# Kernel tuning notes

Hardware: AMD Instinct MI355X
Metric: run time of the kernel (lower is better)

Reference implementation:

```python
import jax, jax.numpy as jnp
import numpy as np

B, S, D, H, MEM, P = 32, 512, 768, 8, 768, 3
DK = D // H
LN_EPS = 1e-6


def _layer_norm(x, a, b):
    # torch LayerNorm in source uses unbiased std (ddof=1) and adds eps to std
    mean = x.mean(-1, keepdims=True)
    var = ((x - mean) ** 2).sum(-1, keepdims=True) / (x.shape[-1] - 1)
    return a * (x - mean) / (jnp.sqrt(var) + LN_EPS) + b


def _gcn_branch(x, mask, Wq, bq, Wk, bk, Ws, bs):
    # x: [B,S,D], mask: [B,S] 0/1 ints
    q = (x @ Wq.T + bq).reshape(B, S, H, DK).transpose(0, 2, 1, 3)  # [B,H,S,DK]
    k = (x @ Wk.T + bk).reshape(B, S, H, DK).transpose(0, 2, 1, 3)
    scores = jnp.einsum('bhqd,bhkd->bhqk', q, k) / jnp.sqrt(jnp.float32(DK))
    scores = jnp.where(mask[:, None, None, :] == 0, jnp.float32(-1e9), scores)
    adj = jax.nn.softmax(scores, axis=-1).mean(1)  # average heads -> [B,S,S]
    # adj - diag(diag(adj)) + I  ==  set diagonal to 1
    idx = jnp.arange(S)
    adj = adj.at[:, idx, idx].set(1.0)
    adj = adj * mask[:, :, None].astype(adj.dtype)  # src_mask.transpose(1,2) * adj
    denom = adj.sum(-1, keepdims=True) + 1.0
    out = x
    for W, b in zip(Ws, bs):
        out = jax.nn.relu((adj @ out @ W.T + b) / denom)
    return out, adj


def _proj(a, b):
    # Proj(a, b): (a.b / |b|) * normalize(b)
    b_mo = jnp.sqrt((b * b).sum(-1))
    axb = (a * b).sum(-1)
    bn = b / jnp.maximum(jnp.sqrt((b * b).sum(-1, keepdims=True)), 1e-12)
    return (axb / b_mo)[:, None] * bn


def setup_inputs() -> dict:
    key = jax.random.key(0)
    ks = jax.random.split(key, 32)

    def w(k, shape):
        return jax.random.normal(k, shape, jnp.float32) * 0.02

    inp = {
        'sequence_output': jax.random.normal(ks[0], (B, S, D), jnp.float32),
        'pooled_output': jax.random.normal(ks[1], (B, D), jnp.float32),
        'src_mask': jnp.ones((B, S), jnp.int32),
        'aspect_mask': jnp.ones((B, S), jnp.float32),
        'ln_a': jnp.ones((D,), jnp.float32),
        'ln_b': jnp.zeros((D,), jnp.float32),
        'fp_Wq': w(ks[2], (D, D)), 'fp_bq': jnp.zeros((D,), jnp.float32),
        'fp_Wk': w(ks[3], (D, D)), 'fp_bk': jnp.zeros((D,), jnp.float32),
        'fp_W0': w(ks[4], (MEM, D)), 'fp_b0': jnp.zeros((MEM,), jnp.float32),
        'fp_W1': w(ks[5], (MEM, MEM)), 'fp_b1': jnp.zeros((MEM,), jnp.float32),
        'fc_Wq': w(ks[6], (D, D)), 'fc_bq': jnp.zeros((D,), jnp.float32),
        'fc_Wk': w(ks[7], (D, D)), 'fc_bk': jnp.zeros((D,), jnp.float32),
        'fc_W0': w(ks[8], (MEM, D)), 'fc_b0': jnp.zeros((MEM,), jnp.float32),
        'fc_W1': w(ks[9], (MEM, MEM)), 'fc_b1': jnp.zeros((MEM,), jnp.float32),
        'fp_dense_W': w(ks[10], (P, MEM)), 'fp_dense_b': jnp.zeros((P,), jnp.float32),
        'fc_dense_W': w(ks[11], (P, MEM)), 'fc_dense_b': jnp.zeros((P,), jnp.float32),
    }
    return inp


def reference(sequence_output, pooled_output, src_mask, aspect_mask,
              ln_a, ln_b,
              fp_Wq, fp_bq, fp_Wk, fp_bk, fp_W0, fp_b0, fp_W1, fp_b1,
              fc_Wq, fc_bq, fc_Wk, fc_bk, fc_W0, fc_b0, fc_W1, fc_b1,
              fp_dense_W, fp_dense_b, fc_dense_W, fc_dense_b):
    label_embedding = pooled_output
    att_inputs = _layer_norm(sequence_output, ln_a, ln_b)  # dropout disabled (eval)
    asp_wn = aspect_mask.sum(1)[:, None]  # [B,1]

    fp_out, _ = _gcn_branch(att_inputs, src_mask, fp_Wq, fp_bq, fp_Wk, fp_bk,
                            [fp_W0, fp_W1], [fp_b0, fp_b1])
    fc_out, _ = _gcn_branch(att_inputs, src_mask, fc_Wq, fc_bq, fc_Wk, fc_bk,
                            [fc_W0, fc_W1], [fc_b0, fc_b1])

    outputs_fp = fp_out.sum(1)  # [B,MEM]
    outputs_fc = (fc_out * aspect_mask[:, :, None]).sum(1) / asp_wn  # [B,MEM]

    fp_x = _proj(outputs_fp, outputs_fc)
    fp_y = _proj(outputs_fp, outputs_fp - fp_x)
    fc_y = outputs_fc  # gradient-reverse layer is identity in forward

    logits_p = fp_y @ fp_dense_W.T + fp_dense_b
    logits_c = fc_y @ fc_dense_W.T + fc_dense_b
    return (logits_p, logits_c, fp_y, label_embedding)
```

## Files before the change

### kernel.cpp

```cpp
#include <hip/hip_runtime.h>
#include <math.h>
#include <stdint.h>

#define Bn 32
#define Sn 512
#define Dn 768
#define Hn 8
#define DKn 96
#define Pn 3

typedef __bf16 bf16_t;
typedef bf16_t bf16x8 __attribute__((ext_vector_type(8)));
typedef float f32x4 __attribute__((ext_vector_type(4)));

__device__ __forceinline__ bf16_t f2bf(float f) { return (bf16_t)f; }

__device__ __forceinline__ void gload16(const void* g, void* l) {
    __builtin_amdgcn_global_load_lds((const __attribute__((address_space(1))) void*)g,
                                     (__attribute__((address_space(3))) void*)l, 16, 0, 0);
}

__device__ __forceinline__ float brsum(float v, float* red) {
    int t = threadIdx.x;
    red[t] = v; __syncthreads();
    #pragma unroll
    for (int o = 128; o > 0; o >>= 1) {
        if (t < o) red[t] += red[t + o];
        __syncthreads();
    }
    float r = red[0]; __syncthreads();
    return r;
}

__global__ __launch_bounds__(256) void ln_kernel(const float* __restrict__ in,
                                                 const float* __restrict__ ga,
                                                 const float* __restrict__ gb,
                                                 bf16_t* __restrict__ out) {
    __shared__ float red[256];
    long row = blockIdx.x;
    const float* x = in + row * Dn;
    bf16_t* y = out + row * Dn;
    int t = threadIdx.x;
    float v0 = x[t], v1 = x[t + 256], v2 = x[t + 512];
    float mean = brsum(v0 + v1 + v2, red) / (float)Dn;
    float d0 = v0 - mean, d1 = v1 - mean, d2 = v2 - mean;
    float ss = brsum(d0 * d0 + d1 * d1 + d2 * d2, red);
    float inv = 1.0f / (sqrtf(ss / (float)(Dn - 1)) + 1e-6f);
    y[t]       = f2bf(ga[t]       * d0 * inv + gb[t]);
    y[t + 256] = f2bf(ga[t + 256] * d1 * inv + gb[t + 256]);
    y[t + 512] = f2bf(ga[t + 512] * d2 * inv + gb[t + 512]);
}

__global__ __launch_bounds__(256) void cvt8(const float* __restrict__ s0,
                                            const float* __restrict__ s1,
                                            const float* __restrict__ s2,
                                            const float* __restrict__ s3,
                                            const float* __restrict__ s4,
                                            const float* __restrict__ s5,
                                            const float* __restrict__ s6,
                                            const float* __restrict__ s7,
                                            bf16_t* __restrict__ dst) {
    int y = blockIdx.y;
    const float* s = (y == 0) ? s0 : (y == 1) ? s1 : (y == 2) ? s2 : (y == 3) ? s3
                   : (y == 4) ? s4 : (y == 5) ? s5 : (y == 6) ? s6 : s7;
    long i = (long)blockIdx.x * 1024 + threadIdx.x * 4;
    float4 v = *reinterpret_cast<const float4*>(s + i);
    bf16_t* d = dst + (long)y * Dn * Dn + i;
    d[0] = f2bf(v.x); d[1] = f2bf(v.y); d[2] = f2bf(v.z); d[3] = f2bf(v.w);
}

__global__ __launch_bounds__(256) void biascat_k(const float* __restrict__ s0,
                                                 const float* __restrict__ s1,
                                                 const float* __restrict__ s2,
                                                 const float* __restrict__ s3,
                                                 const float* __restrict__ s4,
                                                 const float* __restrict__ s5,
                                                 const float* __restrict__ s6,
                                                 const float* __restrict__ s7,
                                                 float* __restrict__ dst) {
    int y = blockIdx.x;
    const float* s = (y == 0) ? s0 : (y == 1) ? s1 : (y == 2) ? s2 : (y == 3) ? s3
                   : (y == 4) ? s4 : (y == 5) ? s5 : (y == 6) ? s6 : s7;
    for (int i = threadIdx.x; i < Dn; i += 256) dst[(long)y * Dn + i] = s[i];
}

__global__ void zero_kernel(float* p, int n) {
    int i = blockIdx.x * 256 + threadIdx.x;
    if (i < n) p[i] = 0.0f;
}

template <int EPI>
__global__ __launch_bounds__(256) void gemm_bt(
    const bf16_t* __restrict__ Ag, const bf16_t* __restrict__ Bg,
    bf16_t* __restrict__ Cg, float* __restrict__ outv,
    int lda, int ldb, int ldc, int K,
    long sAhi, long sAlo, long sBhi, long sBlo, long sChi, long sClo,
    int lgZ, float alpha,
    const float* __restrict__ bias, long bias_zs,
    const float* __restrict__ denom,
    const float* __restrict__ aspw) {
    __shared__ __align__(16) bf16_t As[128 * 32];
    __shared__ __align__(16) bf16_t Bs[128 * 32];

    unsigned gx = gridDim.x, gy = gridDim.y;
    unsigned nwg = gx * gy * gridDim.z;
    unsigned flat = (blockIdx.z * gy + blockIdx.y) * gx + blockIdx.x;
    unsigned q8 = nwg >> 3, r8 = nwg & 7;
    unsigned xcd = flat & 7, idx = flat >> 3;
    unsigned swz = (xcd < r8 ? xcd * (q8 + 1) : r8 * (q8 + 1) + (xcd - r8) * q8) + idx;
    unsigned bx = swz % gx;
    unsigned rest = swz / gx;
    unsigned by = rest % gy;
    unsigned zz = rest / gy;
    int zb = zz >> lgZ;
    int zg = zz & ((1 << lgZ) - 1);
    long zful = zz;

    const bf16_t* A = Ag + zb * sAhi + zg * sAlo;
    const bf16_t* B = Bg + zb * sBhi + zg * sBlo;

    int n0 = bx * 128;
    int m0 = by * 128;
    int tid = threadIdx.x;
    int lane = tid & 63, wv = tid >> 6;
    int wm = wv >> 1, wn = wv & 1;

    int sub = lane >> 2;
    int kcol = (lane & 3) * 8;
    const bf16_t* pA0 = A + (size_t)(m0 + wv * 16 + sub) * lda + kcol;
    const bf16_t* pA1 = pA0 + (size_t)64 * lda;
    const bf16_t* pB0 = B + (size_t)(n0 + wv * 16 + sub) * ldb + kcol;
    const bf16_t* pB1 = pB0 + (size_t)64 * ldb;
    bf16_t* lA0 = As + wv * 512 + lane * 8;
    bf16_t* lA1 = As + (4 + wv) * 512 + lane * 8;
    bf16_t* lB0 = Bs + wv * 512 + lane * 8;
    bf16_t* lB1 = Bs + (4 + wv) * 512 + lane * 8;

    f32x4 acc[4][4];
    #pragma unroll
    for (int i = 0; i < 4; i++)
        #pragma unroll
        for (int j = 0; j < 4; j++) acc[i][j] = (f32x4){0.f, 0.f, 0.f, 0.f};

    const bf16_t* ar = As + (wm * 64 + (lane & 15)) * 32 + (lane >> 4) * 8;
    const bf16_t* br = Bs + (wn * 64 + (lane & 15)) * 32 + (lane >> 4) * 8;

    for (int k0 = 0; k0 < K; k0 += 32) {
        gload16(pA0 + k0, lA0);
        gload16(pA1 + k0, lA1);
        gload16(pB0 + k0, lB0);
        gload16(pB1 + k0, lB1);
        __syncthreads();
        bf16x8 a[4], b[4];
        #pragma unroll
        for (int i = 0; i < 4; i++) a[i] = *(const bf16x8*)(ar + i * 16 * 32);
        #pragma unroll
        for (int j = 0; j < 4; j++) b[j] = *(const bf16x8*)(br + j * 16 * 32);
        #pragma unroll
        for (int i = 0; i < 4; i++)
            #pragma unroll
            for (int j = 0; j < 4; j++)
                acc[i][j] = __builtin_amdgcn_mfma_f32_16x16x32_bf16(a[i], b[j], acc[i][j], 0, 0, 0);
        __syncthreads();
    }

    int nb = n0 + wn * 64 + (lane & 15);
    int mbase = m0 + wm * 64 + (lane >> 4) * 4;
    const float* bz = bias ? bias + zb * bias_zs : nullptr;

    if (EPI == 0) {
        bf16_t* Cz = Cg + zb * sChi + zg * sClo;
        #pragma unroll
        for (int i = 0; i < 4; i++) {
            #pragma unroll
            for (int r = 0; r < 4; r++) {
                long m = mbase + i * 16 + r;
                bf16_t* crow = Cz + m * (long)ldc;
                #pragma unroll
                for (int j = 0; j < 4; j++) {
                    int col = nb + j * 16;
                    float v = acc[i][j][r] * alpha;
                    if (bz) v += bz[col];
                    crow[col] = f2bf(v);
                }
            }
        }
    } else if (EPI == 1) {
        bf16_t* Cz = Cg + zb * sChi + zg * sClo;
        const float* dz = denom + zful * Sn;
        #pragma unroll
        for (int i = 0; i < 4; i++) {
            #pragma unroll
            for (int r = 0; r < 4; r++) {
                int m = mbase + i * 16 + r;
                float dinv = 1.0f / dz[m];
                bf16_t* crow = Cz + (long)m * ldc;
                #pragma unroll
                for (int j = 0; j < 4; j++) {
                    float v = fmaxf((acc[i][j][r] + bz[nb + j * 16]) * dinv, 0.0f);
                    crow[nb + j * 16] = f2bf(v);
                }
            }
        }
    } else {
        const float* dz = denom + zful * Sn;
        float csum[4] = {0.f, 0.f, 0.f, 0.f};
        #pragma unroll
        for (int i = 0; i < 4; i++) {
            #pragma unroll
            for (int r = 0; r < 4; r++) {
                int m = mbase + i * 16 + r;
                float dinv = 1.0f / dz[m];
                float wgt = (aspw && zb) ? aspw[(long)zg * Sn + m] : 1.0f;
                #pragma unroll
                for (int j = 0; j < 4; j++) {
                    float v = fmaxf((acc[i][j][r] + bz[nb + j * 16]) * dinv, 0.0f);
                    csum[j] += v * wgt;
                }
            }
        }
        #pragma unroll
        for (int j = 0; j < 4; j++) {
            float s = csum[j];
            s += __shfl_xor(s, 16);
            s += __shfl_xor(s, 32);
            if (lane < 16) atomicAdd(&outv[zful * Dn + nb + j * 16], s);
        }
    }
}

template <int EPI>
__global__ __launch_bounds__(512, 1) void gemm256(
    const bf16_t* __restrict__ Ag, const bf16_t* __restrict__ Bg,
    bf16_t* __restrict__ Cg, float* __restrict__ outv,
    int lda, int ldb, int ldc, int K,
    long sAhi, long sAlo, long sBhi, long sBlo, long sChi, long sClo,
    int lgZ,
    const float* __restrict__ bias, long bias_zs,
    const float* __restrict__ denom,
    const float* __restrict__ aspw) {
    __shared__ __align__(16) bf16_t lds[4][2][8192];

    unsigned gx = gridDim.x, gy = gridDim.y;
    unsigned nwg = gx * gy * gridDim.z;
    unsigned flat = (blockIdx.z * gy + blockIdx.y) * gx + blockIdx.x;
    unsigned q8 = nwg >> 3, r8 = nwg & 7;
    unsigned xcd = flat & 7, idx = flat >> 3;
    unsigned swz = (xcd < r8 ? xcd * (q8 + 1) : r8 * (q8 + 1) + (xcd - r8) * q8) + idx;
    unsigned bx = swz % gx;
    unsigned rest = swz / gx;
    unsigned by = rest % gy;
    unsigned zz = rest / gy;
    int zb = zz >> lgZ;
    int zg = zz & ((1 << lgZ) - 1);
    long zful = zz;

    const bf16_t* A = Ag + zb * sAhi + zg * sAlo;
    const bf16_t* B = Bg + zb * sBhi + zg * sBlo;

    int n0 = bx * 256, m0 = by * 256;
    int tid = threadIdx.x;
    int lane = tid & 63, w = tid >> 6;
    int wm = w >> 2, wn = w & 3;

    const int NT = K >> 5;

    int srow = lane & 15;
    int skc = (lane >> 4) * 8;
    const bf16_t* Asrc0 = A + (size_t)(m0 + (w * 2 + 0) * 16 + srow) * lda + skc;
    const bf16_t* Asrc1 = A + (size_t)(m0 + (w * 2 + 1) * 16 + srow) * lda + skc;
    const bf16_t* Bsrc0 = B + (size_t)(n0 + (w * 2 + 0) * 16 + srow) * ldb + skc;
    const bf16_t* Bsrc1 = B + (size_t)(n0 + (w * 2 + 1) * 16 + srow) * ldb + skc;
    int c0off = (w * 2 + 0) * 512 + lane * 8;
    int c1off = (w * 2 + 1) * 512 + lane * 8;

    f32x4 acc[8][4];
    #pragma unroll
    for (int i = 0; i < 8; ++i)
        #pragma unroll
        for (int j = 0; j < 4; ++j) acc[i][j] = (f32x4){0.f, 0.f, 0.f, 0.f};

    #pragma unroll
    for (int tt = 0; tt < 3; ++tt) {
        gload16(Asrc0 + tt * 32, &lds[tt][0][c0off]);
        gload16(Asrc1 + tt * 32, &lds[tt][0][c1off]);
        gload16(Bsrc0 + tt * 32, &lds[tt][1][c0off]);
        gload16(Bsrc1 + tt * 32, &lds[tt][1][c1off]);
    }
    asm volatile("s_waitcnt vmcnt(8)" ::: "memory");
    __builtin_amdgcn_s_barrier();

    int aoff = wm * 8 * 512 + lane * 8;
    int boff = wn * 4 * 512 + lane * 8;

    for (int t = 0; t < NT; ++t) {
        const bf16_t* bufA = &lds[t & 3][0][0];
        const bf16_t* bufB = &lds[t & 3][1][0];
        int tn = t + 3;
        bf16_t* dA = &lds[tn & 3][0][0];
        bf16_t* dB = &lds[tn & 3][1][0];
        bool st = tn < NT;

        bf16x8 a[4], b[4];
        #pragma unroll
        for (int i = 0; i < 4; ++i)
            a[i] = *(const bf16x8*)(bufA + aoff + i * 512);
        #pragma unroll
        for (int j = 0; j < 4; ++j)
            b[j] = *(const bf16x8*)(bufB + boff + j * 512);
        if (st) {
            gload16(Asrc0 + tn * 32, dA + c0off);
            gload16(Bsrc0 + tn * 32, dB + c0off);
        }
        __builtin_amdgcn_s_barrier();
        asm volatile("s_waitcnt lgkmcnt(0)" ::: "memory");
        __builtin_amdgcn_sched_barrier(0);
        __builtin_amdgcn_s_setprio(1);
        #pragma unroll
        for (int i = 0; i < 4; ++i)
            #pragma unroll
            for (int j = 0; j < 4; ++j)
                acc[i][j] = __builtin_amdgcn_mfma_f32_16x16x32_bf16(a[i], b[j], acc[i][j], 0, 0, 0);
        __builtin_amdgcn_s_setprio(0);
        __builtin_amdgcn_s_barrier();

        #pragma unroll
        for (int i = 0; i < 4; ++i)
            a[i] = *(const bf16x8*)(bufA + aoff + (4 + i) * 512);
        if (st) {
            gload16(Asrc1 + tn * 32, dA + c1off);
            gload16(Bsrc1 + tn * 32, dB + c1off);
        }
        __builtin_amdgcn_s_barrier();
        asm volatile("s_waitcnt lgkmcnt(0)" ::: "memory");
        __builtin_amdgcn_sched_barrier(0);
        __builtin_amdgcn_s_setprio(1);
        #pragma unroll
        for (int i = 0; i < 4; ++i)
            #pragma unroll
            for (int j = 0; j < 4; ++j)
                acc[4 + i][j] = __builtin_amdgcn_mfma_f32_16x16x32_bf16(a[i], b[j], acc[4 + i][j], 0, 0, 0);
        __builtin_amdgcn_s_setprio(0);
        if (t + 3 < NT)      asm volatile("s_waitcnt vmcnt(8)" ::: "memory");
        else if (t + 2 < NT) asm volatile("s_waitcnt vmcnt(4)" ::: "memory");
        else                 asm volatile("s_waitcnt vmcnt(0)" ::: "memory");
        __builtin_amdgcn_s_barrier();
    }

    int nb = n0 + wn * 64 + (lane & 15);
    int mbase = m0 + wm * 128 + (lane >> 4) * 4;
    const float* bz = bias ? bias + zb * bias_zs : nullptr;

    if (EPI == 0) {
        bf16_t* Cz = Cg + zb * sChi + zg * sClo;
        #pragma unroll
        for (int i = 0; i < 8; ++i) {
            #pragma unroll
            for (int r = 0; r < 4; ++r) {
                long m = mbase + i * 16 + r;
                bf16_t* crow = Cz + m * (long)ldc;
                #pragma unroll
                for (int j = 0; j < 4; ++j) {
                    int col = nb + j * 16;
                    float v = acc[i][j][r];
                    if (bz) v += bz[col];
                    crow[col] = f2bf(v);
                }
            }
        }
    }
}

__global__ __launch_bounds__(256, 2) void fused_adj(
    const bf16_t* __restrict__ QK, bf16_t* __restrict__ adjb,
    float* __restrict__ denomv, const int* __restrict__ mask) {
    __shared__ __align__(16) bf16_t stg[32 * 520];
    __shared__ float red[4][16];

    int L = blockIdx.x;
    int swzi = (L & 7) * 128 + (L >> 3);
    int brc = swzi >> 9;
    int rem = swzi & 511;
    int b = rem >> 4;
    int q0 = (rem & 15) * 32;

    int tid = threadIdx.x;
    int lane = tid & 63, w = tid >> 6;
    int mt = w >> 1, nh = w & 1;
    int g = lane >> 4, c = lane & 15;

    const long LDQ = 3072;
    const bf16_t* Qrow = QK + ((long)b * Sn + q0 + mt * 16 + c) * LDQ + brc * 1536 + g * 8;
    const bf16_t* Kbase = QK + ((long)b * Sn + nh * 64 + c) * LDQ + brc * 1536 + Dn + g * 8;

    const int* mrow = mask + (long)b * Sn;
    unsigned mbits = 0;
    #pragma unroll
    for (int t = 0; t < 4; ++t)
        #pragma unroll
        for (int nj = 0; nj < 4; ++nj)
            if (mrow[t * 128 + nh * 64 + nj * 16 + c] != 0) mbits |= 1u << (t * 4 + nj);

    f32x4 adjacc[4][4];
    #pragma unroll
    for (int t = 0; t < 4; ++t)
        #pragma unroll
        for (int nj = 0; nj < 4; ++nj) adjacc[t][nj] = (f32x4){0.f, 0.f, 0.f, 0.f};

    bf16x8 krA[6], krB[6], aq[3], aqn[3];
    const float sal = 0.102062072615966f;

    #pragma unroll
    for (int jj = 0; jj < 2; ++jj)
        #pragma unroll
        for (int ks = 0; ks < 3; ++ks)
            krA[jj * 3 + ks] = *(const bf16x8*)(Kbase + (long)(jj * 16) * LDQ + ks * 32);
    #pragma unroll
    for (int ks = 0; ks < 3; ++ks)
        aq[ks] = *(const bf16x8*)(Qrow + ks * 32);

    for (int h = 0; h < Hn; ++h) {
        f32x4 S[4][4];
        #pragma unroll
        for (int t = 0; t < 4; ++t)
            #pragma unroll
            for (int nj = 0; nj < 4; ++nj) S[t][nj] = (f32x4){0.f, 0.f, 0.f, 0.f};

        #pragma unroll
        for (int ht = 0; ht < 8; ++ht) {
            const int t = ht >> 1, half = ht & 1;
            const int nht = (ht + 1) & 7;
            const int hinc = (ht == 7) ? 1 : 0;
            const int t2 = nht >> 1, half2 = nht & 1;
            const bf16_t* kb2 = Kbase + (long)(t2 * 128) * LDQ + (long)(h + hinc) * 96;
            if ((ht & 1) == 0) {
                #pragma unroll
                for (int jj = 0; jj < 2; ++jj)
                    #pragma unroll
                    for (int ks = 0; ks < 3; ++ks)
                        krB[jj * 3 + ks] = *(const bf16x8*)(kb2 + (long)((half2 * 2 + jj) * 16) * LDQ + ks * 32);
            } else {
                #pragma unroll
                for (int jj = 0; jj < 2; ++jj)
                    #pragma unroll
                    for (int ks = 0; ks < 3; ++ks)
                        krA[jj * 3 + ks] = *(const bf16x8*)(kb2 + (long)((half2 * 2 + jj) * 16) * LDQ + ks * 32);
            }
            if (ht == 6) {
                #pragma unroll
                for (int ks = 0; ks < 3; ++ks)
                    aqn[ks] = *(const bf16x8*)(Qrow + (long)(h + 1) * 96 + ks * 32);
            }
            if ((ht & 1) == 0) {
                #pragma unroll
                for (int jj = 0; jj < 2; ++jj)
                    #pragma unroll
                    for (int ks = 0; ks < 3; ++ks)
                        S[t][half * 2 + jj] = __builtin_amdgcn_mfma_f32_16x16x32_bf16(
                            aq[ks], krA[jj * 3 + ks], S[t][half * 2 + jj], 0, 0, 0);
            } else {
                #pragma unroll
                for (int jj = 0; jj < 2; ++jj)
                    #pragma unroll
                    for (int ks = 0; ks < 3; ++ks)
                        S[t][half * 2 + jj] = __builtin_amdgcn_mfma_f32_16x16x32_bf16(
                            aq[ks], krB[jj * 3 + ks], S[t][half * 2 + jj], 0, 0, 0);
            }
        }

        float rs[4] = {0.f, 0.f, 0.f, 0.f};
        #pragma unroll
        for (int t = 0; t < 4; ++t)
            #pragma unroll
            for (int nj = 0; nj < 4; ++nj) {
                float mkf = ((mbits >> (t * 4 + nj)) & 1u) ? 1.0f : 0.0f;
                #pragma unroll
                for (int ri = 0; ri < 4; ++ri) {
                    float e = mkf * __expf(S[t][nj][ri] * sal);
                    S[t][nj][ri] = e;
                    rs[ri] += e;
                }
            }
        #pragma unroll
        for (int ri = 0; ri < 4; ++ri) {
            rs[ri] += __shfl_xor(rs[ri], 1);
            rs[ri] += __shfl_xor(rs[ri], 2);
            rs[ri] += __shfl_xor(rs[ri], 4);
            rs[ri] += __shfl_xor(rs[ri], 8);
        }
        if (c == 0) {
            #pragma unroll
            for (int ri = 0; ri < 4; ++ri) red[w][g * 4 + ri] = rs[ri];
        }
        __syncthreads();
        float inv[4];
        #pragma unroll
        for (int ri = 0; ri < 4; ++ri)
            inv[ri] = 0.125f / (red[w][g * 4 + ri] + red[w ^ 1][g * 4 + ri]);
        __syncthreads();
        #pragma unroll
        for (int t = 0; t < 4; ++t)
            #pragma unroll
            for (int nj = 0; nj < 4; ++nj)
                #pragma unroll
                for (int ri = 0; ri < 4; ++ri)
                    adjacc[t][nj][ri] += S[t][nj][ri] * inv[ri];
        if (h < 7) {
            #pragma unroll
            for (int ks = 0; ks < 3; ++ks) aq[ks] = aqn[ks];
        }
    }

    float rm[4];
    #pragma unroll
    for (int ri = 0; ri < 4; ++ri)
        rm[ri] = (mrow[q0 + mt * 16 + g * 4 + ri] != 0) ? 1.0f : 0.0f;
    float rs2[4] = {0.f, 0.f, 0.f, 0.f};
    #pragma unroll
    for (int t = 0; t < 4; ++t)
        #pragma unroll
        for (int nj = 0; nj < 4; ++nj) {
            int n = t * 128 + nh * 64 + nj * 16 + c;
            #pragma unroll
            for (int ri = 0; ri < 4; ++ri) {
                float v = adjacc[t][nj][ri];
                int q = q0 + mt * 16 + g * 4 + ri;
                if (n == q) v = 1.0f;
                v *= rm[ri];
                adjacc[t][nj][ri] = v;
                rs2[ri] += v;
            }
        }
    #pragma unroll
    for (int ri = 0; ri < 4; ++ri) {
        rs2[ri] += __shfl_xor(rs2[ri], 1);
        rs2[ri] += __shfl_xor(rs2[ri], 2);
        rs2[ri] += __shfl_xor(rs2[ri], 4);
        rs2[ri] += __shfl_xor(rs2[ri], 8);
    }
    if (c == 0) {
        #pragma unroll
        for (int ri = 0; ri < 4; ++ri) red[w][g * 4 + ri] = rs2[ri];
    }
    __syncthreads();
    long zful = (long)brc * Bn + b;
    if (nh == 0 && c == 0) {
        #pragma unroll
        for (int ri = 0; ri < 4; ++ri)
            denomv[zful * Sn + q0 + mt * 16 + g * 4 + ri] =
                red[w][g * 4 + ri] + red[w ^ 1][g * 4 + ri] + 1.0f;
    }
    #pragma unroll
    for (int t = 0; t < 4; ++t)
        #pragma unroll
        for (int nj = 0; nj < 4; ++nj) {
            int n = t * 128 + nh * 64 + nj * 16 + c;
            #pragma unroll
            for (int ri = 0; ri < 4; ++ri)
                stg[(mt * 16 + g * 4 + ri) * 520 + n] = f2bf(adjacc[t][nj][ri]);
        }
    __syncthreads();
    bf16_t* arow = adjb + (zful * Sn + q0) * Sn;
    #pragma unroll
    for (int p = 0; p < 8; ++p) {
        int gr = tid + p * 256;
        int row = gr >> 6, cc = gr & 63;
        *(bf16x8*)(arow + (long)row * Sn + cc * 8) = *(const bf16x8*)(stg + row * 520 + cc * 8);
    }
}

__global__ __launch_bounds__(256) void final_kernel(const float* __restrict__ ofp,
                                                    const float* __restrict__ ofc_raw,
                                                    const float* __restrict__ aspect,
                                                    const float* __restrict__ pooled,
                                                    const float* __restrict__ fpdW,
                                                    const float* __restrict__ fpdb,
                                                    const float* __restrict__ fcdW,
                                                    const float* __restrict__ fcdb,
                                                    float* __restrict__ out) {
    __shared__ float red[256];
    __shared__ float fp[Dn], fc[Dn], fy[Dn];
    int b = blockIdx.x, t = threadIdx.x;
    float awv = aspect[(long)b * Sn + t] + aspect[(long)b * Sn + t + 256];
    float asp_wn = brsum(awv, red);
    for (int i = t; i < Dn; i += 256) {
        fp[i] = ofp[(long)b * Dn + i];
        fc[i] = ofc_raw[(long)b * Dn + i] / asp_wn;
    }
    __syncthreads();
    float p0 = 0.0f, p1 = 0.0f;
    for (int i = t; i < Dn; i += 256) { p0 += fc[i] * fc[i]; p1 += fp[i] * fc[i]; }
    float dfc2 = brsum(p0, red);
    float dfpfc = brsum(p1, red);
    float bmo = sqrtf(dfc2);
    float coef = dfpfc / bmo;
    float bden = fmaxf(bmo, 1e-12f);
    float q0 = 0.0f, q1 = 0.0f;
    for (int i = t; i < Dn; i += 256) {
        float tv = fp[i] - coef * fc[i] / bden;
        fy[i] = tv;
        q0 += tv * tv;
        q1 += fp[i] * tv;
    }
    float dt2 = brsum(q0, red);
    float dfpt = brsum(q1, red);
    float tmo = sqrtf(dt2);
    float coef2 = dfpt / tmo;
    float tden = fmaxf(tmo, 1e-12f);
    for (int i = t; i < Dn; i += 256) fy[i] = coef2 * fy[i] / tden;
    __syncthreads();
    for (int i = t; i < Dn; i += 256) out[2 * Bn * Pn + (long)b * Dn + i] = fy[i];
    for (int i = t; i < Dn; i += 256)
        out[2 * Bn * Pn + Bn * Dn + (long)b * Dn + i] = pooled[(long)b * Dn + i];
    for (int j = 0; j < Pn; j++) {
        float lp = 0.0f, lc = 0.0f;
        for (int i = t; i < Dn; i += 256) {
            lp += fy[i] * fpdW[(long)j * Dn + i];
            lc += fc[i] * fcdW[(long)j * Dn + i];
        }
        float rp = brsum(lp, red);
        float rc = brsum(lc, red);
        if (t == 0) {
            out[(long)b * Pn + j] = rp + fpdb[j];
            out[Bn * Pn + (long)b * Pn + j] = rc + fcdb[j];
        }
    }
}

extern "C" void kernel_launch(void* const* d_in, const int* in_sizes, int n_in,
                              void* d_out, int out_size, void* d_ws, size_t ws_size,
                              hipStream_t stream) {
    const float* seq     = (const float*)d_in[0];
    const float* pooled  = (const float*)d_in[1];
    const int*   src_msk = (const int*)d_in[2];
    const float* aspect  = (const float*)d_in[3];
    const float* ln_a    = (const float*)d_in[4];
    const float* ln_b    = (const float*)d_in[5];
    float* out = (float*)d_out;

    const long NTD = (long)Bn * Sn * Dn;
    const long NSS = (long)Bn * Sn * Sn;
    const long DD  = (long)Dn * Dn;
    const long SD  = (long)Sn * Dn;

    char* w = (char*)d_ws;
    bf16_t* xbf   = (bf16_t*)w;
    bf16_t* QK    = xbf + NTD;
    bf16_t* H1    = QK;
    bf16_t* XT    = QK + 2 * NTD;
    bf16_t* adjb  = QK + 4 * NTD;
    float*  denom = (float*)(adjb + 2 * NSS);
    float*  ofp   = denom + 2L * Bn * Sn;
    float*  bcat  = ofp + 2L * Bn * Dn;
    bf16_t* Wb    = (bf16_t*)(bcat + 8 * Dn);

    ln_kernel<<<dim3(Bn * Sn), dim3(256), 0, stream>>>(seq, ln_a, ln_b, xbf);
    zero_kernel<<<dim3((2 * Bn * Dn + 255) / 256), dim3(256), 0, stream>>>(ofp, 2 * Bn * Dn);

    cvt8<<<dim3(576, 8), dim3(256), 0, stream>>>(
        (const float*)d_in[6], (const float*)d_in[8],
        (const float*)d_in[14], (const float*)d_in[16],
        (const float*)d_in[10], (const float*)d_in[18],
        (const float*)d_in[12], (const float*)d_in[20], Wb);
    biascat_k<<<dim3(8), dim3(256), 0, stream>>>(
        (const float*)d_in[7], (const float*)d_in[9],
        (const float*)d_in[15], (const float*)d_in[17],
        (const float*)d_in[11], (const float*)d_in[19],
        (const float*)d_in[13], (const float*)d_in[21], bcat);

    gemm256<0><<<dim3(12, 64, 1), dim3(512), 0, stream>>>(
        xbf, Wb, QK, nullptr, Dn, Dn, 3072, Dn,
        0, 0, 0, 0, 0, 0, 0, bcat, 0, nullptr, nullptr);

    fused_adj<<<dim3(2 * Bn * Sn / 32), dim3(256), 0, stream>>>(QK, adjb, denom, src_msk);

    gemm_bt<0><<<dim3(4, 6, 64), dim3(256), 0, stream>>>(
        Wb + 4 * DD, xbf, XT, nullptr, Dn, Dn, Sn, Dn,
        DD, 0, 0, SD, 32 * SD, SD,
        5, 1.0f, nullptr, 0, nullptr, nullptr);

    gemm_bt<1><<<dim3(6, 4, 64), dim3(256), 0, stream>>>(
        adjb, XT, H1, nullptr, Sn, Sn, Dn, Sn,
        32L * Sn * Sn, (long)Sn * Sn, 32 * SD, SD, 32 * SD, SD,
        5, 1.0f, bcat + 4 * Dn, Dn, denom, nullptr);

    gemm_bt<0><<<dim3(4, 6, 64), dim3(256), 0, stream>>>(
        Wb + 6 * DD, H1, XT, nullptr, Dn, Dn, Sn, Dn,
        DD, 0, 32 * SD, SD, 32 * SD, SD,
        5, 1.0f, nullptr, 0, nullptr, nullptr);

    gemm_bt<2><<<dim3(6, 4, 64), dim3(256), 0, stream>>>(
        adjb, XT, nullptr, ofp, Sn, Sn, 0, Sn,
        32L * Sn * Sn, (long)Sn * Sn, 32 * SD, SD, 0, 0,
        5, 1.0f, bcat + 6 * Dn, Dn, denom, aspect);

    final_kernel<<<dim3(Bn), dim3(256), 0, stream>>>(
        ofp, ofp + (long)Bn * Dn, aspect, pooled,
        (const float*)d_in[22], (const float*)d_in[23],
        (const float*)d_in[24], (const float*)d_in[25], out);
}
```

Before: 566.4 us.

## Stage K tiles through double-buffered LDS in fused_adj with 512-thread blocks

The fused adjacency kernel used to have each wave load its own K fragments straight from global memory into registers. It now loads each 128-row K tile for a head cooperatively into a padded, double-buffered LDS buffer, prefetching two tiles ahead in registers. Blocks grow from 4 to 8 waves, each covering 32 key columns instead of 64, and the row-sum reduction now spans four waves. This is meant to cut redundant global K loads and raise occupancy, at the cost of a __syncthreads per tile and extra LDS traffic.

Result: slower. 654.6 us (median of 3 runs) (+15.6%).

```diff
diff --git a/kernel.cpp b/kernel.cpp
--- a/kernel.cpp
+++ b/kernel.cpp
@@ -253,7 +253,6 @@
     unsigned zz = rest / gy;
     int zb = zz >> lgZ;
     int zg = zz & ((1 << lgZ) - 1);
-    long zful = zz;
 
     const bf16_t* A = Ag + zb * sAhi + zg * sAlo;
     const bf16_t* B = Bg + zb * sBhi + zg * sBlo;
@@ -371,11 +370,11 @@
     }
 }
 
-__global__ __launch_bounds__(256, 2) void fused_adj(
+__global__ __launch_bounds__(512, 4) void fused_adj(
     const bf16_t* __restrict__ QK, bf16_t* __restrict__ adjb,
     float* __restrict__ denomv, const int* __restrict__ mask) {
-    __shared__ __align__(16) bf16_t stg[32 * 520];
-    __shared__ float red[4][16];
+    __shared__ __align__(16) bf16_t shmem[2 * 128 * 100];
+    __shared__ float red[8][16];
 
     int L = blockIdx.x;
     int swzi = (L & 7) * 128 + (L >> 3);
@@ -386,128 +385,139 @@
 
     int tid = threadIdx.x;
     int lane = tid & 63, w = tid >> 6;
-    int mt = w >> 1, nh = w & 1;
+    int mt = w >> 2, nh = w & 3;
     int g = lane >> 4, c = lane & 15;
 
     const long LDQ = 3072;
     const bf16_t* Qrow = QK + ((long)b * Sn + q0 + mt * 16 + c) * LDQ + brc * 1536 + g * 8;
-    const bf16_t* Kbase = QK + ((long)b * Sn + nh * 64 + c) * LDQ + brc * 1536 + Dn + g * 8;
+    const bf16_t* Kst  = QK + (long)b * Sn * LDQ + brc * 1536 + Dn;
 
     const int* mrow = mask + (long)b * Sn;
     unsigned mbits = 0;
     #pragma unroll
     for (int t = 0; t < 4; ++t)
         #pragma unroll
-        for (int nj = 0; nj < 4; ++nj)
-            if (mrow[t * 128 + nh * 64 + nj * 16 + c] != 0) mbits |= 1u << (t * 4 + nj);
-
-    f32x4 adjacc[4][4];
+        for (int grp = 0; grp < 2; ++grp)
+            if (mrow[t * 128 + nh * 32 + grp * 16 + c] != 0) mbits |= 1u << (t * 2 + grp);
+
+    int sr[3], sc[3];
+    #pragma unroll
+    for (int p = 0; p < 3; ++p) { int ci = tid + p * 512; sr[p] = ci / 12; sc[p] = (ci % 12) * 8; }
+
+    bf16_t* Ks0 = shmem;
+    bf16_t* Ks1 = shmem + 128 * 100;
+
+    f32x4 adjacc[4][2];
     #pragma unroll
     for (int t = 0; t < 4; ++t)
         #pragma unroll
-        for (int nj = 0; nj < 4; ++nj) adjacc[t][nj] = (f32x4){0.f, 0.f, 0.f, 0.f};
-
-    bf16x8 krA[6], krB[6], aq[3], aqn[3];
+        for (int grp = 0; grp < 2; ++grp) adjacc[t][grp] = (f32x4){0.f, 0.f, 0.f, 0.f};
+
+    bf16x8 krA[3], krB[3];
     const float sal = 0.102062072615966f;
 
     #pragma unroll
-    for (int jj = 0; jj < 2; ++jj)
+    for (int p = 0; p < 3; ++p)
+        krA[p] = *(const bf16x8*)(Kst + (long)sr[p] * LDQ + sc[p]);
+    #pragma unroll
+    for (int p = 0; p < 3; ++p)
+        *(bf16x8*)(Ks0 + sr[p] * 100 + sc[p]) = krA[p];
+    #pragma unroll
+    for (int p = 0; p < 3; ++p)
+        krB[p] = *(const bf16x8*)(Kst + (long)(128 + sr[p]) * LDQ + sc[p]);
+    __syncthreads();
+
+    int koff = (nh * 32 + c) * 100 + g * 8;
+
+    for (int h = 0; h < Hn; ++h) {
+        f32x4 S[4][2];
+        #pragma unroll
+        for (int t = 0; t < 4; ++t)
+            #pragma unroll
+            for (int grp = 0; grp < 2; ++grp) S[t][grp] = (f32x4){0.f, 0.f, 0.f, 0.f};
+        bf16x8 aq[3];
         #pragma unroll
         for (int ks = 0; ks < 3; ++ks)
-            krA[jj * 3 + ks] = *(const bf16x8*)(Kbase + (long)(jj * 16) * LDQ + ks * 32);
-    #pragma unroll
-    for (int ks = 0; ks < 3; ++ks)
-        aq[ks] = *(const bf16x8*)(Qrow + ks * 32);
-
-    for (int h = 0; h < Hn; ++h) {
-        f32x4 S[4][4];
-        #pragma unroll
-        for (int t = 0; t < 4; ++t)
-            #pragma unroll
-            for (int nj = 0; nj < 4; ++nj) S[t][nj] = (f32x4){0.f, 0.f, 0.f, 0.f};
-
-        #pragma unroll
-        for (int ht = 0; ht < 8; ++ht) {
-            const int t = ht >> 1, half = ht & 1;
-            const int nht = (ht + 1) & 7;
-            const int hinc = (ht == 7) ? 1 : 0;
-            const int t2 = nht >> 1, half2 = nht & 1;
-            const bf16_t* kb2 = Kbase + (long)(t2 * 128) * LDQ + (long)(h + hinc) * 96;
-            if ((ht & 1) == 0) {
-                #pragma unroll
-                for (int jj = 0; jj < 2; ++jj)
+            aq[ks] = *(const bf16x8*)(Qrow + (long)h * 96 + ks * 32);
+
+        #pragma unroll
+        for (int t = 0; t < 4; ++t) {
+            int it = h * 4 + t;
+            if (it + 2 < 32) {
+                int i2 = it + 2, t2 = i2 & 3, h2 = i2 >> 2;
+                const bf16_t* kb = Kst + (long)(t2 * 128) * LDQ + h2 * 96;
+                if ((it & 1) == 0) {
                     #pragma unroll
-                    for (int ks = 0; ks < 3; ++ks)
-                        krB[jj * 3 + ks] = *(const bf16x8*)(kb2 + (long)((half2 * 2 + jj) * 16) * LDQ + ks * 32);
-            } else {
-                #pragma unroll
-                for (int jj = 0; jj < 2; ++jj)
+                    for (int p = 0; p < 3; ++p)
+                        krA[p] = *(const bf16x8*)(kb + (long)sr[p] * LDQ + sc[p]);
+                } else {
                     #pragma unroll
-                    for (int ks = 0; ks < 3; ++ks)
-                        krA[jj * 3 + ks] = *(const bf16x8*)(kb2 + (long)((half2 * 2 + jj) * 16) * LDQ + ks * 32);
-            }
-            if (ht == 6) {
-                #pragma unroll
-                for (int ks = 0; ks < 3; ++ks)
-                    aqn[ks] = *(const bf16x8*)(Qrow + (long)(h + 1) * 96 + ks * 32);
-            }
-            if ((ht & 1) == 0) {
-                #pragma unroll
-                for (int jj = 0; jj < 2; ++jj)
+                    for (int p = 0; p < 3; ++p)
+                        krB[p] = *(const bf16x8*)(kb + (long)sr[p] * LDQ + sc[p]);
+                }
+            }
+            const bf16_t* kbuf = (it & 1) ? Ks1 : Ks0;
+            #pragma unroll
+            for (int grp = 0; grp < 2; ++grp) {
+                #pragma unroll
+                for (int ks = 0; ks < 3; ++ks) {
+                    bf16x8 bk = *(const bf16x8*)(kbuf + koff + grp * 1600 + ks * 32);
+                    S[t][grp] = __builtin_amdgcn_mfma_f32_16x16x32_bf16(aq[ks], bk, S[t][grp], 0, 0, 0);
+                }
+            }
+            if (t == 3) {
+                float rs[4] = {0.f, 0.f, 0.f, 0.f};
+                #pragma unroll
+                for (int tt = 0; tt < 4; ++tt)
                     #pragma unroll
-                    for (int ks = 0; ks < 3; ++ks)
-                        S[t][half * 2 + jj] = __builtin_amdgcn_mfma_f32_16x16x32_bf16(
-                            aq[ks], krA[jj * 3 + ks], S[t][half * 2 + jj], 0, 0, 0);
-            } else {
-                #pragma unroll
-                for (int jj = 0; jj < 2; ++jj)
+                    for (int grp = 0; grp < 2; ++grp) {
+                        float mkf = ((mbits >> (tt * 2 + grp)) & 1u) ? 1.0f : 0.0f;
+                        #pragma unroll
+                        for (int ri = 0; ri < 4; ++ri) {
+                            float e = mkf * __expf(S[tt][grp][ri] * sal);
+                            S[tt][grp][ri] = e;
+                            rs[ri] += e;
+                        }
+                    }
+                #pragma unroll
+                for (int ri = 0; ri < 4; ++ri) {
+                    rs[ri] += __shfl_xor(rs[ri], 1);
+                    rs[ri] += __shfl_xor(rs[ri], 2);
+                    rs[ri] += __shfl_xor(rs[ri], 4);
+                    rs[ri] += __shfl_xor(rs[ri], 8);
+                }
+                if (c == 0) {
                     #pragma unroll
-                    for (int ks = 0; ks < 3; ++ks)
-                        S[t][half * 2 + jj] = __builtin_amdgcn_mfma_f32_16x16x32_bf16(
-                            aq[ks], krB[jj * 3 + ks], S[t][half * 2 + jj], 0, 0, 0);
-            }
-        }
-
-        float rs[4] = {0.f, 0.f, 0.f, 0.f};
-        #pragma unroll
-        for (int t = 0; t < 4; ++t)
-            #pragma unroll
-            for (int nj = 0; nj < 4; ++nj) {
-                float mkf = ((mbits >> (t * 4 + nj)) & 1u) ? 1.0f : 0.0f;
-                #pragma unroll
-                for (int ri = 0; ri < 4; ++ri) {
-                    float e = mkf * __expf(S[t][nj][ri] * sal);
-                    S[t][nj][ri] = e;
-                    rs[ri] += e;
-                }
-            }
-        #pragma unroll
-        for (int ri = 0; ri < 4; ++ri) {
-            rs[ri] += __shfl_xor(rs[ri], 1);
-            rs[ri] += __shfl_xor(rs[ri], 2);
-            rs[ri] += __shfl_xor(rs[ri], 4);
-            rs[ri] += __shfl_xor(rs[ri], 8);
-        }
-        if (c == 0) {
-            #pragma unroll
-            for (int ri = 0; ri < 4; ++ri) red[w][g * 4 + ri] = rs[ri];
-        }
-        __syncthreads();
-        float inv[4];
-        #pragma unroll
-        for (int ri = 0; ri < 4; ++ri)
-            inv[ri] = 0.125f / (red[w][g * 4 + ri] + red[w ^ 1][g * 4 + ri]);
-        __syncthreads();
-        #pragma unroll
-        for (int t = 0; t < 4; ++t)
-            #pragma unroll
-            for (int nj = 0; nj < 4; ++nj)
+                    for (int ri = 0; ri < 4; ++ri) red[w][g * 4 + ri] = rs[ri];
+                }
+            }
+            if (it + 1 < 32) {
+                bf16_t* dbuf = ((it + 1) & 1) ? Ks1 : Ks0;
+                if ((it & 1) == 0) {
+                    #pragma unroll
+                    for (int p = 0; p < 3; ++p)
+                        *(bf16x8*)(dbuf + sr[p] * 100 + sc[p]) = krB[p];
+                } else {
+                    #pragma unroll
+                    for (int p = 0; p < 3; ++p)
+                        *(bf16x8*)(dbuf + sr[p] * 100 + sc[p]) = krA[p];
+                }
+            }
+            __syncthreads();
+            if (t == 3) {
+                float inv[4];
                 #pragma unroll
                 for (int ri = 0; ri < 4; ++ri)
-                    adjacc[t][nj][ri] += S[t][nj][ri] * inv[ri];
-        if (h < 7) {
-            #pragma unroll
-            for (int ks = 0; ks < 3; ++ks) aq[ks] = aqn[ks];
+                    inv[ri] = 0.125f / (red[mt * 4 + 0][g * 4 + ri] + red[mt * 4 + 1][g * 4 + ri] +
+                                        red[mt * 4 + 2][g * 4 + ri] + red[mt * 4 + 3][g * 4 + ri]);
+                #pragma unroll
+                for (int tt = 0; tt < 4; ++tt)
+                    #pragma unroll
+                    for (int grp = 0; grp < 2; ++grp)
+                        #pragma unroll
+                        for (int ri = 0; ri < 4; ++ri)
+                            adjacc[tt][grp][ri] += S[tt][grp][ri] * inv[ri];
+            }
         }
     }
 
@@ -519,15 +529,15 @@
     #pragma unroll
     for (int t = 0; t < 4; ++t)
         #pragma unroll
-        for (int nj = 0; nj < 4; ++nj) {
-            int n = t * 128 + nh * 64 + nj * 16 + c;
+        for (int grp = 0; grp < 2; ++grp) {
+            int n = t * 128 + nh * 32 + grp * 16 + c;
             #pragma unroll
             for (int ri = 0; ri < 4; ++ri) {
-                float v = adjacc[t][nj][ri];
+                float v = adjacc[t][grp][ri];
                 int q = q0 + mt * 16 + g * 4 + ri;
                 if (n == q) v = 1.0f;
                 v *= rm[ri];
-                adjacc[t][nj][ri] = v;
+                adjacc[t][grp][ri] = v;
                 rs2[ri] += v;
             }
         }
@@ -538,6 +548,7 @@
         rs2[ri] += __shfl_xor(rs2[ri], 4);
         rs2[ri] += __shfl_xor(rs2[ri], 8);
     }
+    __syncthreads();
     if (c == 0) {
         #pragma unroll
         for (int ri = 0; ri < 4; ++ri) red[w][g * 4 + ri] = rs2[ri];
@@ -548,22 +559,24 @@
         #pragma unroll
         for (int ri = 0; ri < 4; ++ri)
             denomv[zful * Sn + q0 + mt * 16 + g * 4 + ri] =
-                red[w][g * 4 + ri] + red[w ^ 1][g * 4 + ri] + 1.0f;
-    }
+                red[mt * 4 + 0][g * 4 + ri] + red[mt * 4 + 1][g * 4 + ri] +
+                red[mt * 4 + 2][g * 4 + ri] + red[mt * 4 + 3][g * 4 + ri] + 1.0f;
+    }
+    bf16_t* stg = shmem;
     #pragma unroll
     for (int t = 0; t < 4; ++t)
         #pragma unroll
-        for (int nj = 0; nj < 4; ++nj) {
-            int n = t * 128 + nh * 64 + nj * 16 + c;
+        for (int grp = 0; grp < 2; ++grp) {
+            int n = t * 128 + nh * 32 + grp * 16 + c;
             #pragma unroll
             for (int ri = 0; ri < 4; ++ri)
-                stg[(mt * 16 + g * 4 + ri) * 520 + n] = f2bf(adjacc[t][nj][ri]);
+                stg[(mt * 16 + g * 4 + ri) * 520 + n] = f2bf(adjacc[t][grp][ri]);
         }
     __syncthreads();
     bf16_t* arow = adjb + (zful * Sn + q0) * Sn;
     #pragma unroll
-    for (int p = 0; p < 8; ++p) {
-        int gr = tid + p * 256;
+    for (int p = 0; p < 4; ++p) {
+        int gr = tid + p * 512;
         int row = gr >> 6, cc = gr & 63;
         *(bf16x8*)(arow + (long)row * Sn + cc * 8) = *(const bf16x8*)(stg + row * 520 + cc * 8);
     }
@@ -672,7 +685,7 @@
         xbf, Wb, QK, nullptr, Dn, Dn, 3072, Dn,
         0, 0, 0, 0, 0, 0, 0, bcat, 0, nullptr, nullptr);
 
-    fused_adj<<<dim3(2 * Bn * Sn / 32), dim3(256), 0, stream>>>(QK, adjb, denom, src_msk);
+    fused_adj<<<dim3(2 * Bn * Sn / 32), dim3(512), 0, stream>>>(QK, adjb, denom, src_msk);
 
     gemm_bt<0><<<dim3(4, 6, 64), dim3(256), 0, stream>>>(
         Wb + 4 * DD, xbf, XT, nullptr, Dn, Dn, Sn, Dn,
```

## Stage K tiles through double-buffered LDS in fused_adj instead of per-wave global loads

Applied to the files above, without the earlier changes.

Rewrites the score loop of fused_adj so that each 128-row K tile for a head is loaded cooperatively by the whole block into a padded, double-buffered LDS array, and the waves read their MFMA operands from there. Before, each wave fetched its own K fragments straight from global memory, so the two waves sharing the same key columns loaded them twice. The global load for the tile two steps ahead is issued early to hide latency, and the staging buffer is reused afterwards for output. The cost is a block barrier on every tile step, extra LDS traffic, and dropping the min-2-blocks launch bound, which may lower occupancy.

Result: faster. 507.0 us (-10.5%).

```diff
diff --git a/kernel.cpp b/kernel.cpp
--- a/kernel.cpp
+++ b/kernel.cpp
@@ -253,7 +253,6 @@
     unsigned zz = rest / gy;
     int zb = zz >> lgZ;
     int zg = zz & ((1 << lgZ) - 1);
-    long zful = zz;
 
     const bf16_t* A = Ag + zb * sAhi + zg * sAlo;
     const bf16_t* B = Bg + zb * sBhi + zg * sBlo;
@@ -371,10 +370,11 @@
     }
 }
 
-__global__ __launch_bounds__(256, 2) void fused_adj(
+#define KPAD 100
+__global__ __launch_bounds__(256) void fused_adj(
     const bf16_t* __restrict__ QK, bf16_t* __restrict__ adjb,
     float* __restrict__ denomv, const int* __restrict__ mask) {
-    __shared__ __align__(16) bf16_t stg[32 * 520];
+    __shared__ __align__(16) bf16_t Ks[2][128 * KPAD];
     __shared__ float red[4][16];
 
     int L = blockIdx.x;
@@ -389,9 +389,9 @@
     int mt = w >> 1, nh = w & 1;
     int g = lane >> 4, c = lane & 15;
 
-    const long LDQ = 3072;
-    const bf16_t* Qrow = QK + ((long)b * Sn + q0 + mt * 16 + c) * LDQ + brc * 1536 + g * 8;
-    const bf16_t* Kbase = QK + ((long)b * Sn + nh * 64 + c) * LDQ + brc * 1536 + Dn + g * 8;
+    const int LDQ = 3072;
+    const bf16_t* Qrow  = QK + ((long)b * Sn + q0 + mt * 16 + c) * LDQ + brc * 1536;
+    const bf16_t* Kbase = QK + (long)b * Sn * LDQ + brc * 1536 + Dn;
 
     const int* mrow = mask + (long)b * Sn;
     unsigned mbits = 0;
@@ -401,113 +401,125 @@
         for (int nj = 0; nj < 4; ++nj)
             if (mrow[t * 128 + nh * 64 + nj * 16 + c] != 0) mbits |= 1u << (t * 4 + nj);
 
+    int srow[6], scc[6];
+    #pragma unroll
+    for (int p = 0; p < 6; ++p) { int gr = tid + p * 256; srow[p] = gr / 12; scc[p] = gr % 12; }
+
     f32x4 adjacc[4][4];
     #pragma unroll
     for (int t = 0; t < 4; ++t)
         #pragma unroll
         for (int nj = 0; nj < 4; ++nj) adjacc[t][nj] = (f32x4){0.f, 0.f, 0.f, 0.f};
 
-    bf16x8 krA[6], krB[6], aq[3], aqn[3];
+    f32x4 S[4][4];
+    bf16x8 kr0[6], kr1[6], aq[3], aqn[3];
     const float sal = 0.102062072615966f;
 
     #pragma unroll
-    for (int jj = 0; jj < 2; ++jj)
-        #pragma unroll
-        for (int ks = 0; ks < 3; ++ks)
-            krA[jj * 3 + ks] = *(const bf16x8*)(Kbase + (long)(jj * 16) * LDQ + ks * 32);
+    for (int p = 0; p < 6; ++p)
+        kr0[p] = *(const bf16x8*)(Kbase + (long)srow[p] * LDQ + scc[p] * 8);
     #pragma unroll
     for (int ks = 0; ks < 3; ++ks)
-        aq[ks] = *(const bf16x8*)(Qrow + ks * 32);
+        aq[ks] = *(const bf16x8*)(Qrow + ks * 32 + g * 8);
+    #pragma unroll
+    for (int p = 0; p < 6; ++p)
+        *(bf16x8*)(&Ks[0][srow[p] * KPAD + scc[p] * 8]) = kr0[p];
+    #pragma unroll
+    for (int p = 0; p < 6; ++p)
+        kr1[p] = *(const bf16x8*)(Kbase + (long)(128 + srow[p]) * LDQ + scc[p] * 8);
+    __syncthreads();
 
     for (int h = 0; h < Hn; ++h) {
-        f32x4 S[4][4];
         #pragma unroll
         for (int t = 0; t < 4; ++t)
             #pragma unroll
             for (int nj = 0; nj < 4; ++nj) S[t][nj] = (f32x4){0.f, 0.f, 0.f, 0.f};
 
-        #pragma unroll
-        for (int ht = 0; ht < 8; ++ht) {
-            const int t = ht >> 1, half = ht & 1;
-            const int nht = (ht + 1) & 7;
-            const int hinc = (ht == 7) ? 1 : 0;
-            const int t2 = nht >> 1, half2 = nht & 1;
-            const bf16_t* kb2 = Kbase + (long)(t2 * 128) * LDQ + (long)(h + hinc) * 96;
-            if ((ht & 1) == 0) {
-                #pragma unroll
-                for (int jj = 0; jj < 2; ++jj)
+        float rs[4];
+        #pragma unroll
+        for (int t = 0; t < 4; ++t) {
+            int it = h * 4 + t;
+            if (it + 2 < 32) {
+                int nt = it + 2;
+                const bf16_t* kp = Kbase + (long)((nt & 3) * 128) * LDQ + (nt >> 2) * 96;
+                if ((t & 1) == 0) {
                     #pragma unroll
-                    for (int ks = 0; ks < 3; ++ks)
-                        krB[jj * 3 + ks] = *(const bf16x8*)(kb2 + (long)((half2 * 2 + jj) * 16) * LDQ + ks * 32);
-            } else {
-                #pragma unroll
-                for (int jj = 0; jj < 2; ++jj)
+                    for (int p = 0; p < 6; ++p)
+                        kr0[p] = *(const bf16x8*)(kp + (long)srow[p] * LDQ + scc[p] * 8);
+                } else {
                     #pragma unroll
-                    for (int ks = 0; ks < 3; ++ks)
-                        krA[jj * 3 + ks] = *(const bf16x8*)(kb2 + (long)((half2 * 2 + jj) * 16) * LDQ + ks * 32);
-            }
-            if (ht == 6) {
+                    for (int p = 0; p < 6; ++p)
+                        kr1[p] = *(const bf16x8*)(kp + (long)srow[p] * LDQ + scc[p] * 8);
+                }
+            }
+            if (t == 2 && h < 7) {
                 #pragma unroll
                 for (int ks = 0; ks < 3; ++ks)
-                    aqn[ks] = *(const bf16x8*)(Qrow + (long)(h + 1) * 96 + ks * 32);
-            }
-            if ((ht & 1) == 0) {
-                #pragma unroll
-                for (int jj = 0; jj < 2; ++jj)
+                    aqn[ks] = *(const bf16x8*)(Qrow + (h + 1) * 96 + ks * 32 + g * 8);
+            }
+            #pragma unroll
+            for (int nj = 0; nj < 4; ++nj) {
+                #pragma unroll
+                for (int ks = 0; ks < 3; ++ks) {
+                    bf16x8 bk = *(const bf16x8*)(&Ks[t & 1][(nh * 64 + nj * 16 + c) * KPAD + ks * 32 + g * 8]);
+                    S[t][nj] = __builtin_amdgcn_mfma_f32_16x16x32_bf16(aq[ks], bk, S[t][nj], 0, 0, 0);
+                }
+            }
+            if (t == 3) {
+                rs[0] = rs[1] = rs[2] = rs[3] = 0.f;
+                #pragma unroll
+                for (int tt = 0; tt < 4; ++tt)
                     #pragma unroll
-                    for (int ks = 0; ks < 3; ++ks)
-                        S[t][half * 2 + jj] = __builtin_amdgcn_mfma_f32_16x16x32_bf16(
-                            aq[ks], krA[jj * 3 + ks], S[t][half * 2 + jj], 0, 0, 0);
-            } else {
-                #pragma unroll
-                for (int jj = 0; jj < 2; ++jj)
+                    for (int nj = 0; nj < 4; ++nj) {
+                        float mkf = ((mbits >> (tt * 4 + nj)) & 1u) ? 1.0f : 0.0f;
+                        #pragma unroll
+                        for (int ri = 0; ri < 4; ++ri) {
+                            float e = mkf * __expf(S[tt][nj][ri] * sal);
+                            S[tt][nj][ri] = e;
+                            rs[ri] += e;
+                        }
+                    }
+                #pragma unroll
+                for (int ri = 0; ri < 4; ++ri) {
+                    rs[ri] += __shfl_xor(rs[ri], 1);
+                    rs[ri] += __shfl_xor(rs[ri], 2);
+                    rs[ri] += __shfl_xor(rs[ri], 4);
+                    rs[ri] += __shfl_xor(rs[ri], 8);
+                }
+                if (c == 0) {
                     #pragma unroll
-                    for (int ks = 0; ks < 3; ++ks)
-                        S[t][half * 2 + jj] = __builtin_amdgcn_mfma_f32_16x16x32_bf16(
-                            aq[ks], krB[jj * 3 + ks], S[t][half * 2 + jj], 0, 0, 0);
-            }
-        }
-
-        float rs[4] = {0.f, 0.f, 0.f, 0.f};
-        #pragma unroll
-        for (int t = 0; t < 4; ++t)
-            #pragma unroll
-            for (int nj = 0; nj < 4; ++nj) {
-                float mkf = ((mbits >> (t * 4 + nj)) & 1u) ? 1.0f : 0.0f;
-                #pragma unroll
-                for (int ri = 0; ri < 4; ++ri) {
-                    float e = mkf * __expf(S[t][nj][ri] * sal);
-                    S[t][nj][ri] = e;
-                    rs[ri] += e;
-                }
-            }
-        #pragma unroll
-        for (int ri = 0; ri < 4; ++ri) {
-            rs[ri] += __shfl_xor(rs[ri], 1);
-            rs[ri] += __shfl_xor(rs[ri], 2);
-            rs[ri] += __shfl_xor(rs[ri], 4);
-            rs[ri] += __shfl_xor(rs[ri], 8);
-        }
-        if (c == 0) {
-            #pragma unroll
-            for (int ri = 0; ri < 4; ++ri) red[w][g * 4 + ri] = rs[ri];
-        }
-        __syncthreads();
-        float inv[4];
-        #pragma unroll
-        for (int ri = 0; ri < 4; ++ri)
-            inv[ri] = 0.125f / (red[w][g * 4 + ri] + red[w ^ 1][g * 4 + ri]);
-        __syncthreads();
-        #pragma unroll
-        for (int t = 0; t < 4; ++t)
-            #pragma unroll
-            for (int nj = 0; nj < 4; ++nj)
+                    for (int ri = 0; ri < 4; ++ri) red[w][g * 4 + ri] = rs[ri];
+                }
+            }
+            if (it + 1 < 32) {
+                if ((t & 1) == 0) {
+                    #pragma unroll
+                    for (int p = 0; p < 6; ++p)
+                        *(bf16x8*)(&Ks[1][srow[p] * KPAD + scc[p] * 8]) = kr1[p];
+                } else {
+                    #pragma unroll
+                    for (int p = 0; p < 6; ++p)
+                        *(bf16x8*)(&Ks[0][srow[p] * KPAD + scc[p] * 8]) = kr0[p];
+                }
+            }
+            __syncthreads();
+            if (t == 3) {
+                float inv[4];
                 #pragma unroll
                 for (int ri = 0; ri < 4; ++ri)
-                    adjacc[t][nj][ri] += S[t][nj][ri] * inv[ri];
-        if (h < 7) {
-            #pragma unroll
-            for (int ks = 0; ks < 3; ++ks) aq[ks] = aqn[ks];
+                    inv[ri] = 0.125f / (red[w][g * 4 + ri] + red[w ^ 1][g * 4 + ri]);
+                #pragma unroll
+                for (int tt = 0; tt < 4; ++tt)
+                    #pragma unroll
+                    for (int nj = 0; nj < 4; ++nj)
+                        #pragma unroll
+                        for (int ri = 0; ri < 4; ++ri)
+                            adjacc[tt][nj][ri] += S[tt][nj][ri] * inv[ri];
+                if (h < 7) {
+                    #pragma unroll
+                    for (int ks = 0; ks < 3; ++ks) aq[ks] = aqn[ks];
+                }
+            }
         }
     }
 
@@ -538,6 +550,7 @@
         rs2[ri] += __shfl_xor(rs2[ri], 4);
         rs2[ri] += __shfl_xor(rs2[ri], 8);
     }
+    __syncthreads();
     if (c == 0) {
         #pragma unroll
         for (int ri = 0; ri < 4; ++ri) red[w][g * 4 + ri] = rs2[ri];
@@ -550,6 +563,7 @@
             denomv[zful * Sn + q0 + mt * 16 + g * 4 + ri] =
                 red[w][g * 4 + ri] + red[w ^ 1][g * 4 + ri] + 1.0f;
     }
+    bf16_t* stg = &Ks[0][0];
     #pragma unroll
     for (int t = 0; t < 4; ++t)
         #pragma unroll
```
